# Kernel tuning notes

Hardware: AMD Instinct MI355X
Metric: run time of the kernel (lower is better)

## Reference

```python
import jax, jax.numpy as jnp
import numpy as np

P_BINS = 5
T_BINS = 16
B_BINS = P_BINS * T_BINS  # 80
IN_CH = 16
OUT_CH = 32
N_VERTS = 30000   # mesh vertices (cols of conn)
N_PATCH = 30000   # patches (rows of conn / B)
K_NNZ = 3         # nnz per sparse row (interpolation support)


def setup_inputs() -> dict:
    key = jax.random.key(0)
    k1, k2, k3, k4 = jax.random.split(key, 4)
    x = jax.random.normal(k1, (N_VERTS, IN_CH), dtype=jnp.float32)
    conn_idx = jax.random.randint(k2, (N_PATCH * B_BINS, K_NNZ), 0, N_VERTS, dtype=jnp.int32)
    conn_val = jax.random.uniform(k3, (N_PATCH * B_BINS, K_NNZ), dtype=jnp.float32)
    weights = jax.random.normal(k4, (B_BINS, IN_CH, OUT_CH), dtype=jnp.float32)
    return {"x": x, "conn_idx": conn_idx, "conn_val": conn_val, "weights": weights}


def _rotated_weights(weights):
    # layer_weights[j, :, :, i] = weights[(j + p*i) % B]  -> reshape (B*inp, out*t)
    j = jnp.arange(B_BINS)[:, None]
    i = jnp.arange(T_BINS)[None, :]
    idx = (j + P_BINS * i) % B_BINS                       # (B, t)
    lw = weights[idx]                                     # (B, t, inp, out)
    lw = jnp.transpose(lw, (0, 2, 3, 1))                  # (B, inp, out, t)
    return lw.reshape(B_BINS * IN_CH, OUT_CH * T_BINS)


def reference(x, conn_idx, conn_val, weights):
    # sparse.mm(conn, x): gather K vertex features per bin row and weight-sum
    gathered = jnp.einsum('rk,rkc->rc', conn_val, x[conn_idx])  # (N*B, inp)
    h = gathered.reshape(-1, B_BINS * IN_CH)                    # (N, B*inp)
    lw = _rotated_weights(weights)                              # (B*inp, out*t)
    y = h @ lw                                                  # (N, out*t)
    y = y.reshape(-1, OUT_CH, T_BINS)
    return jnp.max(y, axis=-1)                                  # (N, out)
```

## Files before the change

### kernel.cpp

```cpp
#include <hip/hip_runtime.h>
#include <hip/hip_bf16.h>
#include <stdint.h>

#define NP 30000
#define BBINS 80
#define INCH 16
#define OUTCH 32
#define KDIM 1280
#define NDIM 512
#define KSTEPS 40
#define NROWS (NP * BBINS)

typedef __bf16 bf16x8 __attribute__((ext_vector_type(8)));
typedef __bf16 bf16x4 __attribute__((ext_vector_type(4)));
typedef float f32x4 __attribute__((ext_vector_type(4)));

__device__ __forceinline__ void async_ld16(const void* g, void* l) {
    __builtin_amdgcn_global_load_lds(
        (const __attribute__((address_space(1))) unsigned int*)g,
        (__attribute__((address_space(3))) unsigned int*)l,
        16, 0, 0);
}

__global__ void prep_weights(const float* __restrict__ w, __bf16* __restrict__ pw) {
    int gid = blockIdx.x * 256 + threadIdx.x;
    int e  = gid & 7;
    int qs = (gid >> 3) & 3;
    int n  = (gid >> 5) & 511;
    int kc = gid >> 14;
    int kp = kc * 32 + ((qs ^ ((n >> 1) & 3)) << 3) + e;
    int b = kp >> 4, c = kp & 15;
    int o = n >> 4,  t = n & 15;
    int bid = (b + 5 * t) % BBINS;
    pw[gid] = (__bf16)w[(bid * INCH + c) * OUTCH + o];
}

__global__ __launch_bounds__(256) void gather_h(
    const float* __restrict__ x,
    const int*   __restrict__ cidx,
    const float* __restrict__ cval,
    __bf16* __restrict__ h) {
    const int gid = blockIdx.x * 256 + threadIdx.x;
    const int r = gid >> 2;
    const int q = gid & 3;
    const int r3 = r * 3;
    const int i0 = cidx[r3 + 0], i1 = cidx[r3 + 1], i2 = cidx[r3 + 2];
    const float v0 = cval[r3 + 0], v1 = cval[r3 + 1], v2 = cval[r3 + 2];
    const float4 a = *(const float4*)(x + (size_t)i0 * 16 + q * 4);
    const float4 b = *(const float4*)(x + (size_t)i1 * 16 + q * 4);
    const float4 c = *(const float4*)(x + (size_t)i2 * 16 + q * 4);
    bf16x4 hv;
    hv[0] = (__bf16)(v0 * a.x + v1 * b.x + v2 * c.x);
    hv[1] = (__bf16)(v0 * a.y + v1 * b.y + v2 * c.y);
    hv[2] = (__bf16)(v0 * a.z + v1 * b.z + v2 * c.z);
    hv[3] = (__bf16)(v0 * a.w + v1 * b.w + v2 * c.w);
    *(bf16x4*)((char*)h + (size_t)gid * 8) = hv;
}

__global__ __launch_bounds__(256, 2) void gemm_max(
    const __bf16* __restrict__ h,
    const __bf16* __restrict__ pw,
    float* __restrict__ out) {

    __shared__ __align__(16) __bf16 Alds[128 * 32];
    __shared__ __align__(16) __bf16 Blds[256 * 32];

    const int bid = blockIdx.x;
    const int m    = (bid >> 4) * 8 + (bid & 7);
    const int ncol = (bid >> 3) & 1;
    if (m >= 235) return;
    const int mbase = m * 128;

    const int tid  = threadIdx.x;
    const int lane = tid & 63;
    const int wave = tid >> 6;
    const int wave_mrow = wave >> 1;
    const int wave_ncol = wave & 1;

    const int ml = lane & 15, q = lane >> 4;
    const int f = (ml >> 1) & 3;
    int a_off[4], b_off[8];
#pragma unroll
    for (int i = 0; i < 4; ++i)
        a_off[i] = (wave_mrow * 64 + i * 16 + ml) * 64 + ((q ^ f) << 4);
#pragma unroll
    for (int j = 0; j < 8; ++j) {
        int nl = wave_ncol * 128 + j * 16 + ml;
        b_off[j] = nl * 64 + ((q ^ f) << 4);
    }

    f32x4 acc[4][8];
#pragma unroll
    for (int i = 0; i < 4; ++i)
#pragma unroll
        for (int j = 0; j < 8; ++j)
            acc[i][j] = (f32x4){0.f, 0.f, 0.f, 0.f};

    const char* hB  = (const char*)h;
    const char* pwB = (const char*)pw + ncol * 16384 + tid * 16;
    int rg0 = mbase + (tid >> 2);
    int rg1 = rg0 + 64;
    if (rg0 > NP - 1) rg0 = NP - 1;
    if (rg1 > NP - 1) rg1 = NP - 1;
    const int swz = ((tid & 3) ^ ((tid >> 3) & 3)) * 16;
    const char* aSrc0 = hB + (size_t)rg0 * 2560 + swz;
    const char* aSrc1 = hB + (size_t)rg1 * 2560 + swz;
    char* aDst0 = (char*)Alds + tid * 16;
    char* aDst1 = aDst0 + 4096;
    char* bDst  = (char*)Blds + tid * 16;

    for (int kc = 0; kc < KSTEPS; ++kc) {
        const char* bs = pwB + kc * 32768;
#pragma unroll
        for (int i = 0; i < 4; ++i)
            async_ld16(bs + i * 4096, bDst + i * 4096);
        async_ld16(aSrc0 + kc * 64, aDst0);
        async_ld16(aSrc1 + kc * 64, aDst1);
        __syncthreads();

        bf16x8 af[4], bfr[8];
#pragma unroll
        for (int i = 0; i < 4; ++i)
            af[i] = *(const bf16x8*)((const char*)Alds + a_off[i]);
#pragma unroll
        for (int j = 0; j < 8; ++j)
            bfr[j] = *(const bf16x8*)((const char*)Blds + b_off[j]);
#pragma unroll
        for (int i = 0; i < 4; ++i)
#pragma unroll
            for (int j = 0; j < 8; ++j)
                acc[i][j] = __builtin_amdgcn_mfma_f32_16x16x32_bf16(
                    af[i], bfr[j], acc[i][j], 0, 0, 0);
        __syncthreads();
    }

    const int rgrp = lane >> 4;
    const int tl   = lane & 15;
#pragma unroll
    for (int i = 0; i < 4; ++i) {
#pragma unroll
        for (int j = 0; j < 8; ++j) {
            float v0 = acc[i][j][0], v1 = acc[i][j][1];
            float v2 = acc[i][j][2], v3 = acc[i][j][3];
#pragma unroll
            for (int off = 1; off < 16; off <<= 1) {
                v0 = fmaxf(v0, __shfl_xor(v0, off));
                v1 = fmaxf(v1, __shfl_xor(v1, off));
                v2 = fmaxf(v2, __shfl_xor(v2, off));
                v3 = fmaxf(v3, __shfl_xor(v3, off));
            }
            if (tl == 0) {
                const int o  = ncol * 16 + wave_ncol * 8 + j;
                const int pr = mbase + wave_mrow * 64 + i * 16 + rgrp * 4;
                if (pr + 0 < NP) out[(pr + 0) * 32 + o] = v0;
                if (pr + 1 < NP) out[(pr + 1) * 32 + o] = v1;
                if (pr + 2 < NP) out[(pr + 2) * 32 + o] = v2;
                if (pr + 3 < NP) out[(pr + 3) * 32 + o] = v3;
            }
        }
    }
}

extern "C" void kernel_launch(void* const* d_in, const int* in_sizes, int n_in,
                              void* d_out, int out_size, void* d_ws, size_t ws_size,
                              hipStream_t stream) {
    const float* x    = (const float*)d_in[0];
    const int*   cidx = (const int*)d_in[1];
    const float* cval = (const float*)d_in[2];
    const float* w    = (const float*)d_in[3];
    float* out = (float*)d_out;

    __bf16* pw = (__bf16*)d_ws;
    __bf16* h  = (__bf16*)((char*)d_ws + (2 << 20));

    hipLaunchKernelGGL(prep_weights, dim3(2560), dim3(256), 0, stream, w, pw);
    hipLaunchKernelGGL(gather_h, dim3(NROWS * 4 / 256), dim3(256), 0, stream,
                       x, cidx, cval, h);
    hipLaunchKernelGGL(gemm_max, dim3(480), dim3(256), 0, stream,
                       h, (const __bf16*)pw, out);
}
```

Before: 188.1 us.

## Keep compact weight table in LDS and index rotated weights on the fly

Instead of streaming a fully expanded, rotated 1280x512 bf16 weight matrix from global memory every k-step, the GEMM loads the compact 80x32x16 weight table (80 KB) into LDS once per block and computes the rotated bin index per lane, advancing it by two bins each step. Blocks grow to 512 threads covering all 32 output channels, so the grid shrinks from 480 to 235 blocks and each h row tile is read once rather than twice. This removes the expanded weight prep and most of the global B traffic, at the cost of a large LDS footprint that may limit occupancy, possible LDS bank conflicts from the XOR-swizzled gathers, and fewer blocks than there are CUs.

```diff
diff --git a/kernel.cpp b/kernel.cpp
--- a/kernel.cpp
+++ b/kernel.cpp
@@ -10,6 +10,7 @@
 #define NDIM 512
 #define KSTEPS 40
 #define NROWS (NP * BBINS)
+#define MTILES 235
 
 typedef __bf16 bf16x8 __attribute__((ext_vector_type(8)));
 typedef __bf16 bf16x4 __attribute__((ext_vector_type(4)));
@@ -22,17 +23,12 @@
         16, 0, 0);
 }
 
-__global__ void prep_weights(const float* __restrict__ w, __bf16* __restrict__ pw) {
+__global__ void prep_wc(const float* __restrict__ w, __bf16* __restrict__ wc) {
     int gid = blockIdx.x * 256 + threadIdx.x;
-    int e  = gid & 7;
-    int qs = (gid >> 3) & 3;
-    int n  = (gid >> 5) & 511;
-    int kc = gid >> 14;
-    int kp = kc * 32 + ((qs ^ ((n >> 1) & 3)) << 3) + e;
-    int b = kp >> 4, c = kp & 15;
-    int o = n >> 4,  t = n & 15;
-    int bid = (b + 5 * t) % BBINS;
-    pw[gid] = (__bf16)w[(bid * INCH + c) * OUTCH + o];
+    int c   = gid & 15;
+    int o   = (gid >> 4) & 31;
+    int bid = gid >> 9;
+    wc[gid] = (__bf16)w[(bid * INCH + c) * OUTCH + o];
 }
 
 __global__ __launch_bounds__(256) void gather_h(
@@ -57,37 +53,47 @@
     *(bf16x4*)((char*)h + (size_t)gid * 8) = hv;
 }
 
-__global__ __launch_bounds__(256, 2) void gemm_max(
+__global__ __launch_bounds__(512, 2) void gemm_max(
     const __bf16* __restrict__ h,
-    const __bf16* __restrict__ pw,
+    const __bf16* __restrict__ wc,
     float* __restrict__ out) {
 
+    __shared__ __align__(16) __bf16 Wlds[80 * 32 * 16];
     __shared__ __align__(16) __bf16 Alds[128 * 32];
-    __shared__ __align__(16) __bf16 Blds[256 * 32];
-
-    const int bid = blockIdx.x;
-    const int m    = (bid >> 4) * 8 + (bid & 7);
-    const int ncol = (bid >> 3) & 1;
-    if (m >= 235) return;
-    const int mbase = m * 128;
 
     const int tid  = threadIdx.x;
     const int lane = tid & 63;
     const int wave = tid >> 6;
-    const int wave_mrow = wave >> 1;
-    const int wave_ncol = wave & 1;
+    const int wave_mrow = wave >> 2;
+    const int wave_ncol = wave & 3;
+    const int mbase = blockIdx.x * 128;
+
+    {
+        const char* src = (const char*)wc;
+        char* dst = (char*)Wlds + tid * 16;
+#pragma unroll
+        for (int i = 0; i < 10; ++i) {
+            const int byte = tid * 16 + i * 8192;
+            const int bid  = byte >> 10;
+            async_ld16(src + (byte ^ ((bid & 7) << 4)), dst + i * 8192);
+        }
+    }
 
     const int ml = lane & 15, q = lane >> 4;
-    const int f = (ml >> 1) & 3;
-    int a_off[4], b_off[8];
+    const int f  = (ml >> 1) & 3;
+    int a_off[4];
 #pragma unroll
     for (int i = 0; i < 4; ++i)
         a_off[i] = (wave_mrow * 64 + i * 16 + ml) * 64 + ((q ^ f) << 4);
+
+    const int ch = q & 1;
+    int vj4[8];
 #pragma unroll
     for (int j = 0; j < 8; ++j) {
-        int nl = wave_ncol * 128 + j * 16 + ml;
-        b_off[j] = nl * 64 + ((q ^ f) << 4);
+        const int o = wave_ncol * 8 + j;
+        vj4[j] = (o * 2 + ch) << 4;
     }
+    int bid = (q >> 1) + 5 * ml;
 
     f32x4 acc[4][8];
 #pragma unroll
@@ -96,35 +102,25 @@
         for (int j = 0; j < 8; ++j)
             acc[i][j] = (f32x4){0.f, 0.f, 0.f, 0.f};
 
-    const char* hB  = (const char*)h;
-    const char* pwB = (const char*)pw + ncol * 16384 + tid * 16;
-    int rg0 = mbase + (tid >> 2);
-    int rg1 = rg0 + 64;
-    if (rg0 > NP - 1) rg0 = NP - 1;
-    if (rg1 > NP - 1) rg1 = NP - 1;
+    int rg = mbase + (tid >> 2);
+    if (rg > NP - 1) rg = NP - 1;
     const int swz = ((tid & 3) ^ ((tid >> 3) & 3)) * 16;
-    const char* aSrc0 = hB + (size_t)rg0 * 2560 + swz;
-    const char* aSrc1 = hB + (size_t)rg1 * 2560 + swz;
-    char* aDst0 = (char*)Alds + tid * 16;
-    char* aDst1 = aDst0 + 4096;
-    char* bDst  = (char*)Blds + tid * 16;
+    const char* aSrc = (const char*)h + (size_t)rg * 2560 + swz;
+    char* aDst = (char*)Alds + tid * 16;
 
     for (int kc = 0; kc < KSTEPS; ++kc) {
-        const char* bs = pwB + kc * 32768;
-#pragma unroll
-        for (int i = 0; i < 4; ++i)
-            async_ld16(bs + i * 4096, bDst + i * 4096);
-        async_ld16(aSrc0 + kc * 64, aDst0);
-        async_ld16(aSrc1 + kc * 64, aDst1);
+        async_ld16(aSrc + kc * 64, aDst);
         __syncthreads();
 
         bf16x8 af[4], bfr[8];
 #pragma unroll
         for (int i = 0; i < 4; ++i)
             af[i] = *(const bf16x8*)((const char*)Alds + a_off[i]);
+        const int bidK = bid << 10;
+        const int b74  = (bid & 7) << 4;
 #pragma unroll
         for (int j = 0; j < 8; ++j)
-            bfr[j] = *(const bf16x8*)((const char*)Blds + b_off[j]);
+            bfr[j] = *(const bf16x8*)((const char*)Wlds + (bidK + (vj4[j] ^ b74)));
 #pragma unroll
         for (int i = 0; i < 4; ++i)
 #pragma unroll
@@ -132,6 +128,9 @@
                 acc[i][j] = __builtin_amdgcn_mfma_f32_16x16x32_bf16(
                     af[i], bfr[j], acc[i][j], 0, 0, 0);
         __syncthreads();
+
+        bid += 2;
+        if (bid >= BBINS) bid -= BBINS;
     }
 
     const int rgrp = lane >> 4;
@@ -150,7 +149,7 @@
                 v3 = fmaxf(v3, __shfl_xor(v3, off));
             }
             if (tl == 0) {
-                const int o  = ncol * 16 + wave_ncol * 8 + j;
+                const int o  = wave_ncol * 8 + j;
                 const int pr = mbase + wave_mrow * 64 + i * 16 + rgrp * 4;
                 if (pr + 0 < NP) out[(pr + 0) * 32 + o] = v0;
                 if (pr + 1 < NP) out[(pr + 1) * 32 + o] = v1;
@@ -170,12 +169,12 @@
     const float* w    = (const float*)d_in[3];
     float* out = (float*)d_out;
 
-    __bf16* pw = (__bf16*)d_ws;
+    __bf16* wc = (__bf16*)d_ws;
     __bf16* h  = (__bf16*)((char*)d_ws + (2 << 20));
 
-    hipLaunchKernelGGL(prep_weights, dim3(2560), dim3(256), 0, stream, w, pw);
+    hipLaunchKernelGGL(prep_wc, dim3(160), dim3(256), 0, stream, w, wc);
     hipLaunchKernelGGL(gather_h, dim3(NROWS * 4 / 256), dim3(256), 0, stream,
                        x, cidx, cval, h);
-    hipLaunchKernelGGL(gemm_max, dim3(480), dim3(256), 0, stream,
-                       h, (const __bf16*)pw, out);
+    hipLaunchKernelGGL(gemm_max, dim3(MTILES), dim3(512), 0, stream,
+                       h, (const __bf16*)wc, out);
 }
```

Measured after the change: 185.6 us. About the same (-1.3%).
